# Optimization experiments

Hardware: AMD Instinct MI355X
Metric: run time of the kernel (lower is better)

Reference implementation:

```python
import jax, jax.numpy as jnp
import numpy as np

DISTANCE_THRESHOLD = 100.0  # squared-distance threshold (cdist**2 <= thresh)
NO_CODE_ID = -1


def setup_inputs() -> dict:
    key = jax.random.key(0)
    kx, kc = jax.random.split(key)
    x = jax.random.normal(kx, (2, 1024, 64), dtype=jnp.float32)      # [b, s, d] query tokens
    codes = jax.random.normal(kc, (50000, 64), dtype=jnp.float32)    # [n, d] active code bank
    return {"x": x, "codes": codes}


def reference(x, codes):
    # squared euclidean distances, matching torch.cdist(x, codes) ** 2
    x2 = jnp.sum(x * x, axis=-1, keepdims=True)            # [b, s, 1]
    c2 = jnp.sum(codes * codes, axis=-1)                   # [n]
    cross = jnp.einsum('bsd,nd->bsn', x, codes)            # [b, s, n]
    d2 = jnp.maximum(x2 + c2 - 2.0 * cross, 0.0)           # clamp tiny negatives, cdist >= 0

    within = jnp.any(d2 <= DISTANCE_THRESHOLD, axis=-1)    # [b, s]
    nn_ids = jnp.argmin(d2, axis=-1)                       # [b, s]
    return jnp.where(within, nn_ids, NO_CODE_ID)
```

## Files before the change

kernel.cpp:

```cpp
#include <hip/hip_runtime.h>

#define NTOK   2048
#define DIM    64
#define NCODES 50000
#define THRESH 100.0f
#define BIG    3.0e38f
#define MARGIN 4.0f
#define NBLK   391
#define BM32   1564
#define BM32P  1568
#define NCG    64

typedef __attribute__((ext_vector_type(8)))  __bf16 bf16x8;
typedef __attribute__((ext_vector_type(16))) float  float16;

__device__ __forceinline__ unsigned short f2bf(float f) {
    union { float f; unsigned int u; } v; v.f = f;
    unsigned int r = v.u + 0x7FFF + ((v.u >> 16) & 1);
    return (unsigned short)(r >> 16);
}
__device__ __forceinline__ unsigned int pack2(float a, float b) {
    return (unsigned int)f2bf(a) | ((unsigned int)f2bf(b) << 16);
}

__global__ __launch_bounds__(256)
void nn_prep_kernel(const float* __restrict__ x,
                    unsigned short* __restrict__ xbf,
                    float* __restrict__ x2,
                    float* __restrict__ bm32) {
    int g = blockIdx.x * 256 + threadIdx.x;
    {
        int t = g >> 2;
        bm32[(size_t)t * BM32P + BM32 + (g & 3)] = BIG;
    }
    int row = g >> 2;
    int seg = g & 3;
    const float* src = x + (size_t)row * DIM + seg * 16;
    unsigned short* dst = xbf + (size_t)row * DIM + seg * 16;
    float4 v0 = ((const float4*)src)[0];
    float4 v1 = ((const float4*)src)[1];
    float4 v2 = ((const float4*)src)[2];
    float4 v3 = ((const float4*)src)[3];
    float s = 0.f;
    s = fmaf(v0.x, v0.x, s); s = fmaf(v0.y, v0.y, s);
    s = fmaf(v0.z, v0.z, s); s = fmaf(v0.w, v0.w, s);
    s = fmaf(v1.x, v1.x, s); s = fmaf(v1.y, v1.y, s);
    s = fmaf(v1.z, v1.z, s); s = fmaf(v1.w, v1.w, s);
    s = fmaf(v2.x, v2.x, s); s = fmaf(v2.y, v2.y, s);
    s = fmaf(v2.z, v2.z, s); s = fmaf(v2.w, v2.w, s);
    s = fmaf(v3.x, v3.x, s); s = fmaf(v3.y, v3.y, s);
    s = fmaf(v3.z, v3.z, s); s = fmaf(v3.w, v3.w, s);
    uint4 lo, hi;
    lo.x = pack2(v0.x, v0.y); lo.y = pack2(v0.z, v0.w);
    lo.z = pack2(v1.x, v1.y); lo.w = pack2(v1.z, v1.w);
    hi.x = pack2(v2.x, v2.y); hi.y = pack2(v2.z, v2.w);
    hi.z = pack2(v3.x, v3.y); hi.w = pack2(v3.z, v3.w);
    *(uint4*)dst = lo;
    *(uint4*)(dst + 8) = hi;
    s += __shfl_xor(s, 1);
    s += __shfl_xor(s, 2);
    if (seg == 0) x2[row] = s;
}

__global__ __launch_bounds__(256, 2)
void nn_stageA_kernel(const unsigned short* __restrict__ xbf,
                      const float* __restrict__ codes,
                      float* __restrict__ bm32) {
    __shared__ __bf16 cs[128 * 72];
    __shared__ float  c2s[128];

    const int tid  = threadIdx.x;
    const int w    = tid >> 6;
    const int lane = tid & 63;
    const int l31  = lane & 31;
    const int h    = lane >> 5;
    const int gi   = blockIdx.x;
    const int g0   = 6 * gi + min(gi, 7);
    const int nb   = (gi < 7) ? 7 : 6;
    const int t0   = blockIdx.y * 256;

    bf16x8 bfr[4][2];
#pragma unroll
    for (int s = 0; s < 4; ++s)
#pragma unroll
        for (int nj = 0; nj < 2; ++nj)
            bfr[s][nj] = *(const bf16x8*)&xbf[
                (size_t)(t0 + w * 64 + nj * 32 + l31) * DIM + s * 16 + h * 8];

    uint4 pr[2][2];
    float prc[2];
    auto prefetch = [&](int blk) {
        int n0 = blk * 128;
#pragma unroll
        for (int it = 0; it < 2; ++it) {
            int slot = it * 256 + tid;
            int row = slot >> 2, seg = slot & 3;
            int n = n0 + row;
            float4 f0, f1, f2, f3;
            if (n < NCODES) {
                const float4* p = (const float4*)(codes + (size_t)n * DIM + seg * 16);
                f0 = p[0]; f1 = p[1]; f2 = p[2]; f3 = p[3];
            } else {
                f0 = f1 = f2 = f3 = make_float4(0.f, 0.f, 0.f, 0.f);
            }
            float s = 0.f;
            s = fmaf(f0.x, f0.x, s); s = fmaf(f0.y, f0.y, s);
            s = fmaf(f0.z, f0.z, s); s = fmaf(f0.w, f0.w, s);
            s = fmaf(f1.x, f1.x, s); s = fmaf(f1.y, f1.y, s);
            s = fmaf(f1.z, f1.z, s); s = fmaf(f1.w, f1.w, s);
            s = fmaf(f2.x, f2.x, s); s = fmaf(f2.y, f2.y, s);
            s = fmaf(f2.z, f2.z, s); s = fmaf(f2.w, f2.w, s);
            s = fmaf(f3.x, f3.x, s); s = fmaf(f3.y, f3.y, s);
            s = fmaf(f3.z, f3.z, s); s = fmaf(f3.w, f3.w, s);
            pr[it][0].x = pack2(f0.x, f0.y); pr[it][0].y = pack2(f0.z, f0.w);
            pr[it][0].z = pack2(f1.x, f1.y); pr[it][0].w = pack2(f1.z, f1.w);
            pr[it][1].x = pack2(f2.x, f2.y); pr[it][1].y = pack2(f2.z, f2.w);
            pr[it][1].z = pack2(f3.x, f3.y); pr[it][1].w = pack2(f3.z, f3.w);
            s += __shfl_xor(s, 1);
            s += __shfl_xor(s, 2);
            prc[it] = (n < NCODES) ? s : BIG;
        }
    };
    prefetch(g0);

    for (int t = 0; t < nb; ++t) {
        const int blk = g0 + t;
        __syncthreads();

#pragma unroll
        for (int it = 0; it < 2; ++it) {
            int slot = it * 256 + tid;
            int row = slot >> 2, seg = slot & 3;
            *(uint4*)&cs[row * 72 + seg * 16] = pr[it][0];
            *(uint4*)&cs[row * 72 + seg * 16 + 8] = pr[it][1];
            if (seg == 0) c2s[row] = prc[it];
        }
        if (t + 1 < nb) prefetch(blk + 1);
        __syncthreads();

        float16 acc[4][2];
#pragma unroll
        for (int mi = 0; mi < 4; ++mi) {
#pragma unroll
            for (int g2 = 0; g2 < 4; ++g2) {
                float4 c4 = *(float4*)&c2s[mi * 32 + g2 * 8 + 4 * h];
#pragma unroll
                for (int i = 0; i < 4; ++i) {
                    float iv = -0.5f * ((float*)&c4)[i];
                    acc[mi][0][g2 * 4 + i] = iv;
                    acc[mi][1][g2 * 4 + i] = iv;
                }
            }
        }

#pragma unroll
        for (int s = 0; s < 4; ++s) {
            bf16x8 a[4];
#pragma unroll
            for (int mi = 0; mi < 4; ++mi)
                a[mi] = *(bf16x8*)&cs[(mi * 32 + l31) * 72 + s * 16 + h * 8];
#pragma unroll
            for (int mi = 0; mi < 4; ++mi)
#pragma unroll
                for (int nj = 0; nj < 2; ++nj)
                    acc[mi][nj] = __builtin_amdgcn_mfma_f32_32x32x16_bf16(
                        a[mi], bfr[s][nj], acc[mi][nj], 0, 0, 0);
        }

#pragma unroll
        for (int nj = 0; nj < 2; ++nj) {
#pragma unroll
            for (int mi = 0; mi < 4; ++mi) {
                float m = acc[mi][nj][0];
#pragma unroll
                for (int r = 1; r < 16; ++r) m = fmaxf(m, acc[mi][nj][r]);
                m = fmaxf(m, __shfl_xor(m, 32));
                if (lane < 32) {
                    int token = t0 + w * 64 + nj * 32 + lane;
                    bm32[(size_t)token * BM32P + blk * 4 + mi] = -2.0f * m;
                }
            }
        }
    }
}

__global__ __launch_bounds__(256)
void nn_finalize_kernel(const float* __restrict__ x,
                        const float* __restrict__ codes,
                        const float* __restrict__ x2,
                        const float* __restrict__ bm32,
                        int* __restrict__ out) {
    __shared__ float redf[8];
    __shared__ int   redi[4];
    __shared__ int   queue[BM32P];
    __shared__ int   qcount;
    __shared__ float gshare;

    const int tid  = threadIdx.x;
    const int w    = tid >> 6;
    const int lane = tid & 63;
    const int t    = blockIdx.x;
    const float* bm = bm32 + (size_t)t * BM32P;

    if (tid == 0) qcount = 0;

    float v[7];
    float g = BIG;
#pragma unroll
    for (int k = 0; k < 7; ++k) {
        int b = tid + k * 256;
        v[k] = (b < BM32P) ? bm[b] : BIG;
        g = fminf(g, v[k]);
    }
#pragma unroll
    for (int m = 1; m < 64; m <<= 1) g = fminf(g, __shfl_xor(g, m));
    if (lane == 0) redf[w] = g;
    __syncthreads();
    if (tid == 0)
        gshare = fminf(fminf(redf[0], redf[1]), fminf(redf[2], redf[3])) + MARGIN;
    __syncthreads();
    const float th = gshare;

#pragma unroll
    for (int k = 0; k < 7; ++k) {
        int b = tid + k * 256;
        if (b < BM32P && v[k] <= th) {
            int slot = atomicAdd(&qcount, 1);
            queue[slot] = b;
        }
    }
    __syncthreads();
    const int nq = qcount;

    const int half = lane & 1;
    float4 xh[8];
#pragma unroll
    for (int q = 0; q < 8; ++q)
        xh[q] = *(const float4*)(x + (size_t)t * DIM + half * 32 + q * 4);
    const float x2v = x2[t];

    float bv = BIG;
    int   bi = 0x7fffffff;
    for (int e = w; e < nq; e += 4) {
        int blk = queue[e];
        int n = blk * 32 + (lane >> 1);
        if (n < NCODES) {
            const float4* cp = (const float4*)(codes + (size_t)n * DIM + half * 32);
            float4 c4[8];
#pragma unroll
            for (int q = 0; q < 8; ++q) c4[q] = cp[q];
            float d = 0.f;
#pragma unroll
            for (int q = 0; q < 8; ++q) {
                d = fmaf(xh[q].x, c4[q].x, d);
                d = fmaf(xh[q].y, c4[q].y, d);
                d = fmaf(xh[q].z, c4[q].z, d);
                d = fmaf(xh[q].w, c4[q].w, d);
            }
            d += __shfl_xor(d, 1);
            float sa = 0.f, sb = 0.f;
#pragma unroll
            for (int q = 0; q < 4; ++q) {
                sa = fmaf(c4[q].x, c4[q].x, sa); sa = fmaf(c4[q].y, c4[q].y, sa);
                sa = fmaf(c4[q].z, c4[q].z, sa); sa = fmaf(c4[q].w, c4[q].w, sa);
            }
#pragma unroll
            for (int q = 4; q < 8; ++q) {
                sb = fmaf(c4[q].x, c4[q].x, sb); sb = fmaf(c4[q].y, c4[q].y, sb);
                sb = fmaf(c4[q].z, c4[q].z, sb); sb = fmaf(c4[q].w, c4[q].w, sb);
            }
            float mysum = sa + sb;
            float other = __shfl_xor(mysum, 1);
            float c2v = half ? (other + mysum) : (mysum + other);
            float d2 = fmaxf(fmaf(-2.f, d, x2v + c2v), 0.f);
            if (d2 < bv || (d2 == bv && n < bi)) { bv = d2; bi = n; }
        }
    }
#pragma unroll
    for (int m = 1; m < 64; m <<= 1) {
        float vv = __shfl_xor(bv, m);
        int   ii = __shfl_xor(bi, m);
        if (vv < bv || (vv == bv && ii < bi)) { bv = vv; bi = ii; }
    }
    if (lane == 0) { redf[4 + w] = bv; redi[w] = bi; }
    __syncthreads();
    if (tid == 0) {
        float fb = BIG;
        int   fi = 0x7fffffff;
#pragma unroll
        for (int i = 0; i < 4; ++i) {
            float vv = redf[4 + i];
            int   ii = redi[i];
            if (vv < fb || (vv == fb && ii < fi)) { fb = vv; fi = ii; }
        }
        out[t] = (fb <= THRESH) ? fi : -1;
    }
}

extern "C" void kernel_launch(void* const* d_in, const int* in_sizes, int n_in,
                              void* d_out, int out_size, void* d_ws, size_t ws_size,
                              hipStream_t stream) {
    const float* x     = (const float*)d_in[0];
    const float* codes = (const float*)d_in[1];

    float* x2 = (float*)d_ws;
    unsigned short* xbf = (unsigned short*)(x2 + NTOK);
    float* bm32 = (float*)(xbf + (size_t)NTOK * DIM);
    int* out = (int*)d_out;

    nn_prep_kernel<<<32, 256, 0, stream>>>(x, xbf, x2, bm32);
    nn_stageA_kernel<<<dim3(NCG, 8), 256, 0, stream>>>(xbf, codes, bm32);
    nn_finalize_kernel<<<NTOK, 256, 0, stream>>>(x, codes, x2, bm32, out);
}
```

Measured before the change: 112.8 us.

## Keep code tiles in registers and stream tokens; fold code norms into MFMA

Stage A drops its shared-memory staging of code tiles. Each block now holds one 128-code tile as bf16 MFMA A-fragments in registers and streams 1024 tokens through it, double-buffering the token fragments. The -0.5*|c|^2 bias is now injected by an extra MFMA whose operand pairs a bf16 code-norm value with a -0.5 constant, replacing the per-element accumulator initialisation. The grid changes from 64x8 to 391x2, the per-token block maxima are written with one float4 store, and the padding initialisation in prep is removed, with finalize now reading only the valid entries. Rounding the code norm to bf16 loses precision, so the coarse-filter MARGIN is raised from 4 to 5 to compensate, which may send more candidate blocks to the exact rescoring step.

```diff
diff --git a/kernel.cpp b/kernel.cpp
--- a/kernel.cpp
+++ b/kernel.cpp
@@ -5,11 +5,10 @@
 #define NCODES 50000
 #define THRESH 100.0f
 #define BIG    3.0e38f
-#define MARGIN 4.0f
+#define MARGIN 5.0f
 #define NBLK   391
 #define BM32   1564
 #define BM32P  1568
-#define NCG    64
 
 typedef __attribute__((ext_vector_type(8)))  __bf16 bf16x8;
 typedef __attribute__((ext_vector_type(16))) float  float16;
@@ -26,13 +25,8 @@
 __global__ __launch_bounds__(256)
 void nn_prep_kernel(const float* __restrict__ x,
                     unsigned short* __restrict__ xbf,
-                    float* __restrict__ x2,
-                    float* __restrict__ bm32) {
+                    float* __restrict__ x2) {
     int g = blockIdx.x * 256 + threadIdx.x;
-    {
-        int t = g >> 2;
-        bm32[(size_t)t * BM32P + BM32 + (g & 3)] = BIG;
-    }
     int row = g >> 2;
     int seg = g & 3;
     const float* src = x + (size_t)row * DIM + seg * 16;
@@ -66,121 +60,89 @@
 void nn_stageA_kernel(const unsigned short* __restrict__ xbf,
                       const float* __restrict__ codes,
                       float* __restrict__ bm32) {
-    __shared__ __bf16 cs[128 * 72];
-    __shared__ float  c2s[128];
-
     const int tid  = threadIdx.x;
     const int w    = tid >> 6;
     const int lane = tid & 63;
     const int l31  = lane & 31;
     const int h    = lane >> 5;
-    const int gi   = blockIdx.x;
-    const int g0   = 6 * gi + min(gi, 7);
-    const int nb   = (gi < 7) ? 7 : 6;
-    const int t0   = blockIdx.y * 256;
-
-    bf16x8 bfr[4][2];
-#pragma unroll
-    for (int s = 0; s < 4; ++s)
-#pragma unroll
-        for (int nj = 0; nj < 2; ++nj)
-            bfr[s][nj] = *(const bf16x8*)&xbf[
-                (size_t)(t0 + w * 64 + nj * 32 + l31) * DIM + s * 16 + h * 8];
-
-    uint4 pr[2][2];
-    float prc[2];
-    auto prefetch = [&](int blk) {
-        int n0 = blk * 128;
-#pragma unroll
-        for (int it = 0; it < 2; ++it) {
-            int slot = it * 256 + tid;
-            int row = slot >> 2, seg = slot & 3;
-            int n = n0 + row;
-            float4 f0, f1, f2, f3;
-            if (n < NCODES) {
-                const float4* p = (const float4*)(codes + (size_t)n * DIM + seg * 16);
-                f0 = p[0]; f1 = p[1]; f2 = p[2]; f3 = p[3];
-            } else {
-                f0 = f1 = f2 = f3 = make_float4(0.f, 0.f, 0.f, 0.f);
-            }
-            float s = 0.f;
-            s = fmaf(f0.x, f0.x, s); s = fmaf(f0.y, f0.y, s);
-            s = fmaf(f0.z, f0.z, s); s = fmaf(f0.w, f0.w, s);
-            s = fmaf(f1.x, f1.x, s); s = fmaf(f1.y, f1.y, s);
-            s = fmaf(f1.z, f1.z, s); s = fmaf(f1.w, f1.w, s);
-            s = fmaf(f2.x, f2.x, s); s = fmaf(f2.y, f2.y, s);
-            s = fmaf(f2.z, f2.z, s); s = fmaf(f2.w, f2.w, s);
-            s = fmaf(f3.x, f3.x, s); s = fmaf(f3.y, f3.y, s);
-            s = fmaf(f3.z, f3.z, s); s = fmaf(f3.w, f3.w, s);
-            pr[it][0].x = pack2(f0.x, f0.y); pr[it][0].y = pack2(f0.z, f0.w);
-            pr[it][0].z = pack2(f1.x, f1.y); pr[it][0].w = pack2(f1.z, f1.w);
-            pr[it][1].x = pack2(f2.x, f2.y); pr[it][1].y = pack2(f2.z, f2.w);
-            pr[it][1].z = pack2(f3.x, f3.y); pr[it][1].w = pack2(f3.z, f3.w);
-            s += __shfl_xor(s, 1);
-            s += __shfl_xor(s, 2);
-            prc[it] = (n < NCODES) ? s : BIG;
-        }
-    };
-    prefetch(g0);
-
-    for (int t = 0; t < nb; ++t) {
-        const int blk = g0 + t;
-        __syncthreads();
-
-#pragma unroll
-        for (int it = 0; it < 2; ++it) {
-            int slot = it * 256 + tid;
-            int row = slot >> 2, seg = slot & 3;
-            *(uint4*)&cs[row * 72 + seg * 16] = pr[it][0];
-            *(uint4*)&cs[row * 72 + seg * 16 + 8] = pr[it][1];
-            if (seg == 0) c2s[row] = prc[it];
-        }
-        if (t + 1 < nb) prefetch(blk + 1);
-        __syncthreads();
-
-        float16 acc[4][2];
+    const int blk  = blockIdx.x;
+    const int n0   = blk * 128;
+    const int tb0  = blockIdx.y * 1024;
+
+    bf16x8 afr[4][4];
+    bf16x8 ac2[4];
+#pragma unroll
+    for (int mi = 0; mi < 4; ++mi) {
+        int row = n0 + mi * 32 + l31;
+        bool valid = row < NCODES;
+        float s2 = 0.f;
+#pragma unroll
+        for (int s = 0; s < 4; ++s) {
+            float4 a = make_float4(0.f, 0.f, 0.f, 0.f), b = a;
+            if (valid) {
+                const float4* p = (const float4*)(codes + (size_t)row * DIM + s * 16 + h * 8);
+                a = p[0]; b = p[1];
+            }
+            s2 = fmaf(a.x, a.x, s2); s2 = fmaf(a.y, a.y, s2);
+            s2 = fmaf(a.z, a.z, s2); s2 = fmaf(a.w, a.w, s2);
+            s2 = fmaf(b.x, b.x, s2); s2 = fmaf(b.y, b.y, s2);
+            s2 = fmaf(b.z, b.z, s2); s2 = fmaf(b.w, b.w, s2);
+            uint4 pk;
+            pk.x = pack2(a.x, a.y); pk.y = pack2(a.z, a.w);
+            pk.z = pack2(b.x, b.y); pk.w = pack2(b.z, b.w);
+            afr[mi][s] = *(bf16x8*)&pk;
+        }
+        s2 += __shfl_xor(s2, 32);
+        float c2v = valid ? s2 : BIG;
+        uint4 uc = make_uint4(0u, 0u, 0u, 0u);
+        if (h == 0) uc.x = (unsigned)f2bf(c2v);
+        ac2[mi] = *(bf16x8*)&uc;
+    }
+    uint4 ub = make_uint4(0u, 0u, 0u, 0u);
+    if (h == 0) ub.x = 0xBF00u;
+    const bf16x8 bc2 = *(bf16x8*)&ub;
+    float16 z16;
+#pragma unroll
+    for (int i = 0; i < 16; ++i) z16[i] = 0.f;
+
+    const unsigned short* xw = xbf + (size_t)(tb0 + w * 32 + l31) * DIM + h * 8;
+    bf16x8 bcur[4], bnxt[4];
+#pragma unroll
+    for (int s = 0; s < 4; ++s) bcur[s] = *(const bf16x8*)(xw + s * 16);
+
+#pragma unroll
+    for (int t = 0; t < 8; ++t) {
+        if (t < 7) {
+            const unsigned short* xn = xw + (size_t)(t + 1) * 128 * DIM;
+#pragma unroll
+            for (int s = 0; s < 4; ++s) bnxt[s] = *(const bf16x8*)(xn + s * 16);
+        }
+        float16 acc[4];
+#pragma unroll
+        for (int mi = 0; mi < 4; ++mi)
+            acc[mi] = __builtin_amdgcn_mfma_f32_32x32x16_bf16(ac2[mi], bc2, z16, 0, 0, 0);
+#pragma unroll
+        for (int s = 0; s < 4; ++s)
+#pragma unroll
+            for (int mi = 0; mi < 4; ++mi)
+                acc[mi] = __builtin_amdgcn_mfma_f32_32x32x16_bf16(
+                    afr[mi][s], bcur[s], acc[mi], 0, 0, 0);
+
+        float4 o;
 #pragma unroll
         for (int mi = 0; mi < 4; ++mi) {
-#pragma unroll
-            for (int g2 = 0; g2 < 4; ++g2) {
-                float4 c4 = *(float4*)&c2s[mi * 32 + g2 * 8 + 4 * h];
-#pragma unroll
-                for (int i = 0; i < 4; ++i) {
-                    float iv = -0.5f * ((float*)&c4)[i];
-                    acc[mi][0][g2 * 4 + i] = iv;
-                    acc[mi][1][g2 * 4 + i] = iv;
-                }
-            }
-        }
-
-#pragma unroll
-        for (int s = 0; s < 4; ++s) {
-            bf16x8 a[4];
-#pragma unroll
-            for (int mi = 0; mi < 4; ++mi)
-                a[mi] = *(bf16x8*)&cs[(mi * 32 + l31) * 72 + s * 16 + h * 8];
-#pragma unroll
-            for (int mi = 0; mi < 4; ++mi)
-#pragma unroll
-                for (int nj = 0; nj < 2; ++nj)
-                    acc[mi][nj] = __builtin_amdgcn_mfma_f32_32x32x16_bf16(
-                        a[mi], bfr[s][nj], acc[mi][nj], 0, 0, 0);
-        }
-
-#pragma unroll
-        for (int nj = 0; nj < 2; ++nj) {
-#pragma unroll
-            for (int mi = 0; mi < 4; ++mi) {
-                float m = acc[mi][nj][0];
-#pragma unroll
-                for (int r = 1; r < 16; ++r) m = fmaxf(m, acc[mi][nj][r]);
-                m = fmaxf(m, __shfl_xor(m, 32));
-                if (lane < 32) {
-                    int token = t0 + w * 64 + nj * 32 + lane;
-                    bm32[(size_t)token * BM32P + blk * 4 + mi] = -2.0f * m;
-                }
-            }
-        }
+            float m = acc[mi][0];
+#pragma unroll
+            for (int r = 1; r < 16; ++r) m = fmaxf(m, acc[mi][r]);
+            m = fmaxf(m, __shfl_xor(m, 32));
+            ((float*)&o)[mi] = -2.0f * m;
+        }
+        if (lane < 32) {
+            int token = tb0 + t * 128 + w * 32 + l31;
+            *(float4*)&bm32[(size_t)token * BM32P + blk * 4] = o;
+        }
+#pragma unroll
+        for (int s = 0; s < 4; ++s) bcur[s] = bnxt[s];
     }
 }
 
@@ -209,7 +171,7 @@
 #pragma unroll
     for (int k = 0; k < 7; ++k) {
         int b = tid + k * 256;
-        v[k] = (b < BM32P) ? bm[b] : BIG;
+        v[k] = (b < BM32) ? bm[b] : BIG;
         g = fminf(g, v[k]);
     }
 #pragma unroll
@@ -224,7 +186,7 @@
 #pragma unroll
     for (int k = 0; k < 7; ++k) {
         int b = tid + k * 256;
-        if (b < BM32P && v[k] <= th) {
+        if (b < BM32 && v[k] <= th) {
             int slot = atomicAdd(&qcount, 1);
             queue[slot] = b;
         }
@@ -308,7 +270,7 @@
     float* bm32 = (float*)(xbf + (size_t)NTOK * DIM);
     int* out = (int*)d_out;
 
-    nn_prep_kernel<<<32, 256, 0, stream>>>(x, xbf, x2, bm32);
-    nn_stageA_kernel<<<dim3(NCG, 8), 256, 0, stream>>>(xbf, codes, bm32);
+    nn_prep_kernel<<<32, 256, 0, stream>>>(x, xbf, x2);
+    nn_stageA_kernel<<<dim3(NBLK, 2), 256, 0, stream>>>(xbf, codes, bm32);
     nn_finalize_kernel<<<NTOK, 256, 0, stream>>>(x, codes, x2, bm32, out);
 }
```

New measurement: 122.4 us. +8.5%, slower.

## Remove prep kernel by fusing bf16 conversion and norm computation into consumers

Applied to the files above, without the earlier changes.

Drops the separate prep launch. Stage A now reads fp32 x directly and packs it to bf16 in registers, and the finalize kernel computes each token's squared norm from the x values it already loads. The per-block max results are stored as a single float4 per token instead of four scalar stores, and the padding entries are skipped by bounding reads at BM32. This removes one kernel launch and its workspace traffic, at the cost of some redundant conversion work across stage-A blocks.

```diff
diff --git a/kernel.cpp b/kernel.cpp
--- a/kernel.cpp
+++ b/kernel.cpp
@@ -23,47 +23,8 @@
     return (unsigned int)f2bf(a) | ((unsigned int)f2bf(b) << 16);
 }
 
-__global__ __launch_bounds__(256)
-void nn_prep_kernel(const float* __restrict__ x,
-                    unsigned short* __restrict__ xbf,
-                    float* __restrict__ x2,
-                    float* __restrict__ bm32) {
-    int g = blockIdx.x * 256 + threadIdx.x;
-    {
-        int t = g >> 2;
-        bm32[(size_t)t * BM32P + BM32 + (g & 3)] = BIG;
-    }
-    int row = g >> 2;
-    int seg = g & 3;
-    const float* src = x + (size_t)row * DIM + seg * 16;
-    unsigned short* dst = xbf + (size_t)row * DIM + seg * 16;
-    float4 v0 = ((const float4*)src)[0];
-    float4 v1 = ((const float4*)src)[1];
-    float4 v2 = ((const float4*)src)[2];
-    float4 v3 = ((const float4*)src)[3];
-    float s = 0.f;
-    s = fmaf(v0.x, v0.x, s); s = fmaf(v0.y, v0.y, s);
-    s = fmaf(v0.z, v0.z, s); s = fmaf(v0.w, v0.w, s);
-    s = fmaf(v1.x, v1.x, s); s = fmaf(v1.y, v1.y, s);
-    s = fmaf(v1.z, v1.z, s); s = fmaf(v1.w, v1.w, s);
-    s = fmaf(v2.x, v2.x, s); s = fmaf(v2.y, v2.y, s);
-    s = fmaf(v2.z, v2.z, s); s = fmaf(v2.w, v2.w, s);
-    s = fmaf(v3.x, v3.x, s); s = fmaf(v3.y, v3.y, s);
-    s = fmaf(v3.z, v3.z, s); s = fmaf(v3.w, v3.w, s);
-    uint4 lo, hi;
-    lo.x = pack2(v0.x, v0.y); lo.y = pack2(v0.z, v0.w);
-    lo.z = pack2(v1.x, v1.y); lo.w = pack2(v1.z, v1.w);
-    hi.x = pack2(v2.x, v2.y); hi.y = pack2(v2.z, v2.w);
-    hi.z = pack2(v3.x, v3.y); hi.w = pack2(v3.z, v3.w);
-    *(uint4*)dst = lo;
-    *(uint4*)(dst + 8) = hi;
-    s += __shfl_xor(s, 1);
-    s += __shfl_xor(s, 2);
-    if (seg == 0) x2[row] = s;
-}
-
 __global__ __launch_bounds__(256, 2)
-void nn_stageA_kernel(const unsigned short* __restrict__ xbf,
+void nn_stageA_kernel(const float* __restrict__ x,
                       const float* __restrict__ codes,
                       float* __restrict__ bm32) {
     __shared__ __bf16 cs[128 * 72];
@@ -83,9 +44,15 @@
 #pragma unroll
     for (int s = 0; s < 4; ++s)
 #pragma unroll
-        for (int nj = 0; nj < 2; ++nj)
-            bfr[s][nj] = *(const bf16x8*)&xbf[
-                (size_t)(t0 + w * 64 + nj * 32 + l31) * DIM + s * 16 + h * 8];
+        for (int nj = 0; nj < 2; ++nj) {
+            const float4* p = (const float4*)(
+                x + (size_t)(t0 + w * 64 + nj * 32 + l31) * DIM + s * 16 + h * 8);
+            float4 a = p[0], b = p[1];
+            uint4 pk;
+            pk.x = pack2(a.x, a.y); pk.y = pack2(a.z, a.w);
+            pk.z = pack2(b.x, b.y); pk.w = pack2(b.z, b.w);
+            bfr[s][nj] = *(bf16x8*)&pk;
+        }
 
     uint4 pr[2][2];
     float prc[2];
@@ -169,16 +136,18 @@
 
 #pragma unroll
         for (int nj = 0; nj < 2; ++nj) {
+            float4 o;
 #pragma unroll
             for (int mi = 0; mi < 4; ++mi) {
                 float m = acc[mi][nj][0];
 #pragma unroll
                 for (int r = 1; r < 16; ++r) m = fmaxf(m, acc[mi][nj][r]);
                 m = fmaxf(m, __shfl_xor(m, 32));
-                if (lane < 32) {
-                    int token = t0 + w * 64 + nj * 32 + lane;
-                    bm32[(size_t)token * BM32P + blk * 4 + mi] = -2.0f * m;
-                }
+                ((float*)&o)[mi] = -2.0f * m;
+            }
+            if (lane < 32) {
+                int token = t0 + w * 64 + nj * 32 + lane;
+                *(float4*)&bm32[(size_t)token * BM32P + blk * 4] = o;
             }
         }
     }
@@ -187,7 +156,6 @@
 __global__ __launch_bounds__(256)
 void nn_finalize_kernel(const float* __restrict__ x,
                         const float* __restrict__ codes,
-                        const float* __restrict__ x2,
                         const float* __restrict__ bm32,
                         int* __restrict__ out) {
     __shared__ float redf[8];
@@ -209,7 +177,7 @@
 #pragma unroll
     for (int k = 0; k < 7; ++k) {
         int b = tid + k * 256;
-        v[k] = (b < BM32P) ? bm[b] : BIG;
+        v[k] = (b < BM32) ? bm[b] : BIG;
         g = fminf(g, v[k]);
     }
 #pragma unroll
@@ -224,7 +192,7 @@
 #pragma unroll
     for (int k = 0; k < 7; ++k) {
         int b = tid + k * 256;
-        if (b < BM32P && v[k] <= th) {
+        if (b < BM32 && v[k] <= th) {
             int slot = atomicAdd(&qcount, 1);
             queue[slot] = b;
         }
@@ -237,7 +205,24 @@
 #pragma unroll
     for (int q = 0; q < 8; ++q)
         xh[q] = *(const float4*)(x + (size_t)t * DIM + half * 32 + q * 4);
-    const float x2v = x2[t];
+
+    float x2v;
+    {
+        float sa = 0.f, sb = 0.f;
+#pragma unroll
+        for (int q = 0; q < 4; ++q) {
+            sa = fmaf(xh[q].x, xh[q].x, sa); sa = fmaf(xh[q].y, xh[q].y, sa);
+            sa = fmaf(xh[q].z, xh[q].z, sa); sa = fmaf(xh[q].w, xh[q].w, sa);
+        }
+#pragma unroll
+        for (int q = 4; q < 8; ++q) {
+            sb = fmaf(xh[q].x, xh[q].x, sb); sb = fmaf(xh[q].y, xh[q].y, sb);
+            sb = fmaf(xh[q].z, xh[q].z, sb); sb = fmaf(xh[q].w, xh[q].w, sb);
+        }
+        float mysum = sa + sb;
+        float other = __shfl_xor(mysum, 1);
+        x2v = half ? (other + mysum) : (mysum + other);
+    }
 
     float bv = BIG;
     int   bi = 0x7fffffff;
@@ -303,12 +288,9 @@
     const float* x     = (const float*)d_in[0];
     const float* codes = (const float*)d_in[1];
 
-    float* x2 = (float*)d_ws;
-    unsigned short* xbf = (unsigned short*)(x2 + NTOK);
-    float* bm32 = (float*)(xbf + (size_t)NTOK * DIM);
+    float* bm32 = (float*)d_ws;
     int* out = (int*)d_out;
 
-    nn_prep_kernel<<<32, 256, 0, stream>>>(x, xbf, x2, bm32);
-    nn_stageA_kernel<<<dim3(NCG, 8), 256, 0, stream>>>(xbf, codes, bm32);
-    nn_finalize_kernel<<<NTOK, 256, 0, stream>>>(x, codes, x2, bm32, out);
-}
+    nn_stageA_kernel<<<dim3(NCG, 8), 256, 0, stream>>>(x, codes, bm32);
+    nn_finalize_kernel<<<NTOK, 256, 0, stream>>>(x, codes, bm32, out);
+}
```

New measurement: 108.6 us. 1.04x faster.
